# Kernel tuning notes

Hardware: AMD Instinct MI355X
Metric: run time of the kernel (lower is better)

The kernel has to match this reference:

```python
import jax, jax.numpy as jnp
import numpy as np

# Mamba defaults (mamba_ssm): d_state=16, d_conv=4, expand=2
D_MODEL = 256
D_STATE = 16
D_CONV = 4
D_INNER = 2 * D_MODEL          # expand * d_model = 512
DT_RANK = (D_MODEL + 15) // 16  # ceil(d_model/16) = 16
BATCH = 8
SEQLEN = 4096
LN_EPS = 1e-5


def setup_inputs() -> dict:
    key = jax.random.key(0)
    ks = jax.random.split(key, 8)
    s = lambda k, shape, sc=0.02: (jax.random.normal(k, shape, jnp.float32) * sc)
    return {
        "x": jax.random.normal(ks[0], (BATCH, SEQLEN, D_MODEL), jnp.float32),
        "in_proj_w": s(ks[1], (2 * D_INNER, D_MODEL)),
        "conv_w": s(ks[2], (D_INNER, 1, D_CONV), 0.1),
        "conv_b": jnp.zeros((D_INNER,), jnp.float32),
        "x_proj_w": s(ks[3], (DT_RANK + 2 * D_STATE, D_INNER)),
        "dt_proj_w": s(ks[4], (D_INNER, DT_RANK), 0.1),
        "dt_proj_b": s(ks[5], (D_INNER,), 0.1),
        "A_log": jnp.log(jnp.broadcast_to(
            jnp.arange(1, D_STATE + 1, dtype=jnp.float32), (D_INNER, D_STATE))),
        "D": jnp.ones((D_INNER,), jnp.float32),
        "out_proj_w": s(ks[6], (D_MODEL, D_INNER)),
        "ln_g": jnp.ones((D_MODEL,), jnp.float32),
        "ln_b": jnpps if False else jnp.zeros((D_MODEL,), jnp.float32),
    }


def _mamba_block(x, in_proj_w, conv_w, conv_b, x_proj_w, dt_proj_w, dt_proj_b,
                 A_log, D, out_proj_w, ln_g, ln_b):
    Bsz = x.shape[0]
    residual = x
    # input projection -> (u, z), each (B, L, d_inner)
    xz = jnp.einsum('bld,ed->ble', x, in_proj_w)
    u, z = jnp.split(xz, 2, axis=-1)
    # causal depthwise conv1d over time, then SiLU
    u_t = jnp.transpose(u, (0, 2, 1))                       # (B, d_inner, L)
    u_pad = jnp.pad(u_t, ((0, 0), (0, 0), (D_CONV - 1, 0)))
    u_conv = jax.lax.conv_general_dilated(
        u_pad, conv_w, window_strides=(1,), padding='VALID',
        feature_group_count=D_INNER) + conv_b[None, :, None]
    u_c = jax.nn.silu(jnp.transpose(u_conv, (0, 2, 1)))     # (B, L, d_inner)
    # input-dependent SSM parameters
    x_dbl = jnp.einsum('bld,ed->ble', u_c, x_proj_w)        # (B, L, dt_rank+2*d_state)
    dt, Bm, Cm = jnp.split(x_dbl, [DT_RANK, DT_RANK + D_STATE], axis=-1)
    delta = jax.nn.softplus(
        jnp.einsum('blr,dr->bld', dt, dt_proj_w) + dt_proj_b)  # (B, L, d_inner)
    A = -jnp.exp(A_log)                                     # (d_inner, d_state)

    def step(state, inputs):
        d_t, B_t, C_t, ut = inputs                          # (B,d_inner),(B,ds),(B,ds),(B,d_inner)
        dA = jnp.exp(d_t[..., None] * A)                    # (B, d_inner, d_state)
        state = state * dA + (d_t * ut)[..., None] * B_t[:, None, :]
        y_t = jnp.einsum('bds,bs->bd', state, C_t)
        return state, y_t

    init = jnp.zeros((Bsz, D_INNER, D_STATE), x.dtype)
    xs = (jnp.moveaxis(delta, 1, 0), jnp.moveaxis(Bm, 1, 0),
          jnp.moveaxis(Cm, 1, 0), jnp.moveaxis(u_c, 1, 0))
    _, ys = jax.lax.scan(step, init, xs)                    # (L, B, d_inner)
    y = jnp.moveaxis(ys, 0, 1) + u_c * D                    # skip term D*u
    y = y * jax.nn.silu(z)                                  # gating
    out = jnp.einsum('bld,ed->ble', y, out_proj_w)          # (B, L, d_model)
    # residual + LayerNorm (dropout is identity in eval)
    h = out + residual
    mu = jnp.mean(h, axis=-1, keepdims=True)
    var = jnp.var(h, axis=-1, keepdims=True)
    return (h - mu) * jax.lax.rsqrt(var + LN_EPS) * ln_g + ln_b


def reference(x, in_proj_w, conv_w, conv_b, x_proj_w, dt_proj_w, dt_proj_b,
              A_log, D, out_proj_w, ln_g, ln_b):
    return _mamba_block(x, in_proj_w, conv_w, conv_b, x_proj_w, dt_proj_w,
                        dt_proj_b, A_log, D, out_proj_w, ln_g, ln_b)
```

## Files before the change

### kernel.cpp

```cpp
#include <hip/hip_runtime.h>

typedef __bf16 bf16x8 __attribute__((ext_vector_type(8)));
typedef __bf16 bf16x4 __attribute__((ext_vector_type(4)));
typedef float f32x4 __attribute__((ext_vector_type(4)));

#define NC 128
#define CL 32

__global__ __launch_bounds__(256) void precomp_a2(
    const float* __restrict__ alog, float* __restrict__ A2)
{
  int i = blockIdx.x * 256 + threadIdx.x;
  int s = i >> 9, d = i & 511;
  A2[i] = -__expf(alog[d * 16 + s]) * 1.44269504f;
}

__global__ __launch_bounds__(256) void gemm_in(
    const float* __restrict__ A, const float* __restrict__ W,
    __bf16* __restrict__ o0, __bf16* __restrict__ o1,
    int K, int split, int ldo)
{
  __shared__ alignas(16) __bf16 lA[128 * 40];
  __shared__ alignas(16) __bf16 lB[128 * 40];
  const int tid  = threadIdx.x;
  const int m0   = blockIdx.x * 128;
  const int n0   = blockIdx.y * 128;
  const int wave = tid >> 6, lane = tid & 63;
  const int wr = (wave & 1) * 64, wc = (wave >> 1) * 64;
  const int fr = lane & 15, kh = (lane >> 4) * 8;
  const int srow = tid >> 3;
  const int skq  = (tid & 7) * 4;

  f32x4 acc[4][4] = {};

  for (int kt = 0; kt < K; kt += 32) {
    __syncthreads();
#pragma unroll
    for (int i = 0; i < 4; ++i) {
      int row = srow + i * 32;
      float4 va = *reinterpret_cast<const float4*>(A + (size_t)(m0 + row) * K + kt + skq);
      float4 vb = *reinterpret_cast<const float4*>(W + (size_t)(n0 + row) * K + kt + skq);
      bf16x4 pa = { (__bf16)va.x, (__bf16)va.y, (__bf16)va.z, (__bf16)va.w };
      bf16x4 pb = { (__bf16)vb.x, (__bf16)vb.y, (__bf16)vb.z, (__bf16)vb.w };
      *reinterpret_cast<bf16x4*>(&lA[row * 40 + skq]) = pa;
      *reinterpret_cast<bf16x4*>(&lB[row * 40 + skq]) = pb;
    }
    __syncthreads();
    bf16x8 af[4], bfr[4];
#pragma unroll
    for (int i = 0; i < 4; ++i) {
      af[i]  = *reinterpret_cast<const bf16x8*>(&lA[(wr + i * 16 + fr) * 40 + kh]);
      bfr[i] = *reinterpret_cast<const bf16x8*>(&lB[(wc + i * 16 + fr) * 40 + kh]);
    }
#pragma unroll
    for (int i = 0; i < 4; ++i)
#pragma unroll
      for (int j = 0; j < 4; ++j)
        acc[i][j] = __builtin_amdgcn_mfma_f32_16x16x32_bf16(af[i], bfr[j], acc[i][j], 0, 0, 0);
  }

  const int cr = (lane >> 4) * 4, cc = lane & 15;
#pragma unroll
  for (int i = 0; i < 4; ++i)
#pragma unroll
    for (int j = 0; j < 4; ++j)
#pragma unroll
      for (int r = 0; r < 4; ++r) {
        int m = m0 + wr + i * 16 + cr + r;
        int n = n0 + wc + j * 16 + cc;
        float v = acc[i][j][r];
        if (n < split) o0[(size_t)m * ldo + n] = (__bf16)v;
        else           o1[(size_t)m * ldo + (n - split)] = (__bf16)v;
      }
}

__global__ __launch_bounds__(256) void gemm_a16(
    const __bf16* __restrict__ A, const float* __restrict__ W,
    float* __restrict__ o)
{
  __shared__ alignas(16) __bf16 lA[128 * 40];
  __shared__ alignas(16) __bf16 lB[128 * 40];
  const int tid  = threadIdx.x;
  const int m0   = blockIdx.x * 128;
  const int n0   = blockIdx.y * 128;
  const int wave = tid >> 6, lane = tid & 63;
  const int wr = (wave & 1) * 64, wc = (wave >> 1) * 64;
  const int fr = lane & 15, kh = (lane >> 4) * 8;
  const int K = 512;

  f32x4 acc[4][4] = {};

  for (int kt = 0; kt < K; kt += 32) {
    __syncthreads();
#pragma unroll
    for (int i = 0; i < 2; ++i) {
      int row = (tid >> 2) + i * 64;
      int sk8 = (tid & 3) * 8;
      *reinterpret_cast<bf16x8*>(&lA[row * 40 + sk8]) =
          *reinterpret_cast<const bf16x8*>(A + (size_t)(m0 + row) * K + kt + sk8);
    }
#pragma unroll
    for (int i = 0; i < 4; ++i) {
      int row = (tid >> 3) + i * 32;
      int sk4 = (tid & 7) * 4;
      float4 vb = *reinterpret_cast<const float4*>(W + (size_t)(n0 + row) * K + kt + sk4);
      bf16x4 pb = { (__bf16)vb.x, (__bf16)vb.y, (__bf16)vb.z, (__bf16)vb.w };
      *reinterpret_cast<bf16x4*>(&lB[row * 40 + sk4]) = pb;
    }
    __syncthreads();
    bf16x8 af[4], bfr[4];
#pragma unroll
    for (int i = 0; i < 4; ++i) {
      af[i]  = *reinterpret_cast<const bf16x8*>(&lA[(wr + i * 16 + fr) * 40 + kh]);
      bfr[i] = *reinterpret_cast<const bf16x8*>(&lB[(wc + i * 16 + fr) * 40 + kh]);
    }
#pragma unroll
    for (int i = 0; i < 4; ++i)
#pragma unroll
      for (int j = 0; j < 4; ++j)
        acc[i][j] = __builtin_amdgcn_mfma_f32_16x16x32_bf16(af[i], bfr[j], acc[i][j], 0, 0, 0);
  }

  const int cr = (lane >> 4) * 4, cc = lane & 15;
#pragma unroll
  for (int i = 0; i < 4; ++i)
#pragma unroll
    for (int j = 0; j < 4; ++j)
#pragma unroll
      for (int r = 0; r < 4; ++r) {
        int m = m0 + wr + i * 16 + cr + r;
        int n = n0 + wc + j * 16 + cc;
        o[(size_t)m * 256 + n] = acc[i][j][r];
      }
}

__global__ __launch_bounds__(256) void gemm_n48(
    const __bf16* __restrict__ A, const float* __restrict__ W, float* __restrict__ o)
{
  __shared__ alignas(16) __bf16 lA[128 * 40];
  __shared__ alignas(16) __bf16 lB[48 * 40];
  const int tid  = threadIdx.x;
  const int m0   = blockIdx.x * 128;
  const int wave = tid >> 6, lane = tid & 63;
  const int wr = wave * 32;
  const int fr = lane & 15, kh = (lane >> 4) * 8;
  const int K = 512;

  f32x4 acc[2][3] = {};

  for (int kt = 0; kt < K; kt += 32) {
    __syncthreads();
#pragma unroll
    for (int i = 0; i < 2; ++i) {
      int row = (tid >> 2) + i * 64;
      int sk8 = (tid & 3) * 8;
      *reinterpret_cast<bf16x8*>(&lA[row * 40 + sk8]) =
          *reinterpret_cast<const bf16x8*>(A + (size_t)(m0 + row) * K + kt + sk8);
    }
#pragma unroll
    for (int i = 0; i < 2; ++i) {
      int slot = tid + i * 256;
      if (slot < 384) {
        int row = slot >> 3, kq = (slot & 7) * 4;
        float4 vb = *reinterpret_cast<const float4*>(W + (size_t)row * K + kt + kq);
        bf16x4 pb = { (__bf16)vb.x, (__bf16)vb.y, (__bf16)vb.z, (__bf16)vb.w };
        *reinterpret_cast<bf16x4*>(&lB[row * 40 + kq]) = pb;
      }
    }
    __syncthreads();
    bf16x8 af[2], bfr[3];
#pragma unroll
    for (int i = 0; i < 2; ++i)
      af[i] = *reinterpret_cast<const bf16x8*>(&lA[(wr + i * 16 + fr) * 40 + kh]);
#pragma unroll
    for (int j = 0; j < 3; ++j)
      bfr[j] = *reinterpret_cast<const bf16x8*>(&lB[(j * 16 + fr) * 40 + kh]);
#pragma unroll
    for (int i = 0; i < 2; ++i)
#pragma unroll
      for (int j = 0; j < 3; ++j)
        acc[i][j] = __builtin_amdgcn_mfma_f32_16x16x32_bf16(af[i], bfr[j], acc[i][j], 0, 0, 0);
  }

  const int cr = (lane >> 4) * 4, cc = lane & 15;
#pragma unroll
  for (int i = 0; i < 2; ++i)
#pragma unroll
    for (int j = 0; j < 3; ++j)
#pragma unroll
      for (int r = 0; r < 4; ++r) {
        int m = m0 + wr + i * 16 + cr + r;
        int n = j * 16 + cc;
        o[(size_t)m * 48 + n] = acc[i][j][r];
      }
}

__global__ __launch_bounds__(256) void conv_silu(
    const __bf16* __restrict__ u, const float* __restrict__ cw,
    const float* __restrict__ cb, __bf16* __restrict__ uc)
{
  int gid = blockIdx.x * 256 + threadIdx.x;
  int d8 = (gid & 63) * 8;
  int q  = gid >> 6;
  int t0 = (q & 1023) * 4;
  int b  = q >> 10;
  size_t base = ((size_t)b * 4096 + t0) * 512 + d8;
  float w0[8], w1[8], w2[8], w3[8], bias[8];
#pragma unroll
  for (int j = 0; j < 8; ++j) {
    float4 wv = *reinterpret_cast<const float4*>(cw + (d8 + j) * 4);
    w0[j] = wv.x; w1[j] = wv.y; w2[j] = wv.z; w3[j] = wv.w;
  }
  *reinterpret_cast<float4*>(&bias[0]) = *reinterpret_cast<const float4*>(cb + d8);
  *reinterpret_cast<float4*>(&bias[4]) = *reinterpret_cast<const float4*>(cb + d8 + 4);
  float x0[8], x1[8], x2[8];
#pragma unroll
  for (int j = 0; j < 8; ++j) { x0[j] = 0.f; x1[j] = 0.f; x2[j] = 0.f; }
  if (t0 > 0) {
    bf16x8 a = *reinterpret_cast<const bf16x8*>(u + base - 3 * 512);
    bf16x8 b2 = *reinterpret_cast<const bf16x8*>(u + base - 2 * 512);
    bf16x8 c = *reinterpret_cast<const bf16x8*>(u + base - 1 * 512);
#pragma unroll
    for (int j = 0; j < 8; ++j) { x0[j] = (float)a[j]; x1[j] = (float)b2[j]; x2[j] = (float)c[j]; }
  }
#pragma unroll
  for (int i = 0; i < 4; ++i) {
    bf16x8 v = *reinterpret_cast<const bf16x8*>(u + base + (size_t)i * 512);
    bf16x8 o;
#pragma unroll
    for (int j = 0; j < 8; ++j) {
      float x3 = (float)v[j];
      float a = fmaf(x3, w3[j], fmaf(x2[j], w2[j], fmaf(x1[j], w1[j], fmaf(x0[j], w0[j], bias[j]))));
      o[j] = (__bf16)(a / (1.f + __expf(-a)));
      x0[j] = x1[j]; x1[j] = x2[j]; x2[j] = x3;
    }
    *reinterpret_cast<bf16x8*>(uc + base + (size_t)i * 512) = o;
  }
}

__global__ __launch_bounds__(256) void scan_p1(
    const float* __restrict__ xdbl, const float* __restrict__ A2t,
    const float* __restrict__ dtw, const float* __restrict__ dtb,
    const float* __restrict__ Dv,
    __bf16* uc ,
    __bf16* __restrict__ cumb, float* __restrict__ hloc)
{
  const int bc = blockIdx.x;
  const int d  = blockIdx.y * 256 + threadIdx.x;
  const size_t row0 = (size_t)bc * CL;
  __shared__ float XD[CL * 48];
  for (int i = threadIdx.x; i < CL * 48; i += 256)
    XD[i] = xdbl[row0 * 48 + i];
  float w[16];
#pragma unroll
  for (int r = 0; r < 4; ++r) {
    float4 t4 = *reinterpret_cast<const float4*>(dtw + d * 16 + r * 4);
    w[r * 4] = t4.x; w[r * 4 + 1] = t4.y; w[r * 4 + 2] = t4.z; w[r * 4 + 3] = t4.w;
  }
  const float A2b  = A2t[d];
  const float bias = dtb[d];
  const float Dd   = Dv[d];
  __syncthreads();
  float st[16];
#pragma unroll
  for (int s = 0; s < 16; ++s) st[s] = 0.f;
  float cum = 0.f;
  for (int t = 0; t < CL; ++t) {
    size_t idx = (row0 + t) * 512 + d;
    float uv = (float)uc[idx];
    float a = bias;
#pragma unroll
    for (int r = 0; r < 16; ++r) a = fmaf(XD[t * 48 + r], w[r], a);
    float dl = fmaxf(a, 0.f) + __logf(1.f + __expf(-fabsf(a)));
    cum += dl;
    cumb[idx] = (__bf16)cum;
    float du = dl * uv;
    float r1 = __builtin_amdgcn_exp2f(dl * A2b);
    float r2 = r1 * r1;
    float r4 = r2 * r2;
    float e0 = r1, e1 = r2, e2 = r2 * r1, e3 = r4;
    float y0 = 0.f, y1 = 0.f, y2 = 0.f, y3 = 0.f;
#pragma unroll
    for (int sg = 0; sg < 4; ++sg) {
      int s0 = sg * 4;
      st[s0 + 0] = fmaf(st[s0 + 0], e0, du * XD[t * 48 + 16 + s0 + 0]);
      y0 = fmaf(st[s0 + 0], XD[t * 48 + 32 + s0 + 0], y0);
      st[s0 + 1] = fmaf(st[s0 + 1], e1, du * XD[t * 48 + 16 + s0 + 1]);
      y1 = fmaf(st[s0 + 1], XD[t * 48 + 32 + s0 + 1], y1);
      st[s0 + 2] = fmaf(st[s0 + 2], e2, du * XD[t * 48 + 16 + s0 + 2]);
      y2 = fmaf(st[s0 + 2], XD[t * 48 + 32 + s0 + 2], y2);
      st[s0 + 3] = fmaf(st[s0 + 3], e3, du * XD[t * 48 + 16 + s0 + 3]);
      y3 = fmaf(st[s0 + 3], XD[t * 48 + 32 + s0 + 3], y3);
      if (sg < 3) { e0 *= r4; e1 *= r4; e2 *= r4; e3 *= r4; }
    }
    uc[idx] = (__bf16)fmaf(uv, Dd, (y0 + y1) + (y2 + y3));
  }
#pragma unroll
  for (int s = 0; s < 16; ++s)
    hloc[((size_t)bc * 16 + s) * 512 + d] = st[s];
}

__global__ __launch_bounds__(256) void scan_p2(
    const float* __restrict__ A2t, const __bf16* __restrict__ cumb,
    float* hloc)
{
  int gt = blockIdx.x * 256 + threadIdx.x;
  int d = gt & 511, s = (gt >> 9) & 15, b = gt >> 13;
  float As2 = A2t[s * 512 + d];
  float st = 0.f;
  for (int c = 0; c < NC; ++c) {
    size_t bc = (size_t)b * NC + c;
    size_t hidx = (bc * 16 + s) * 512 + d;
    float h = hloc[hidx];
    hloc[hidx] = st;
    float ctot = (float)cumb[(bc * CL + CL - 1) * 512 + d];
    st = fmaf(st, __builtin_amdgcn_exp2f(As2 * ctot), h);
  }
}

__global__ __launch_bounds__(256) void scan_p3(
    const __bf16* __restrict__ z, const __bf16* __restrict__ cumb,
    const float* __restrict__ xdbl, const float* __restrict__ A2t,
    const float* __restrict__ sin_,
    __bf16* y )
{
  const int bc = blockIdx.x;
  const int d  = blockIdx.y * 256 + threadIdx.x;
  const size_t row0 = (size_t)bc * CL;
  __shared__ float Csh[CL * 16];
  for (int i = threadIdx.x; i < CL * 16; i += 256) {
    int tt = i >> 4, s = i & 15;
    Csh[i] = xdbl[(row0 + tt) * 48 + 32 + s];
  }
  const float A2b = A2t[d];
  float sn[16];
#pragma unroll
  for (int s = 0; s < 16; ++s) sn[s] = sin_[((size_t)bc * 16 + s) * 512 + d];
  __syncthreads();
  for (int t = 0; t < CL; ++t) {
    size_t idx = (row0 + t) * 512 + d;
    float cum = (float)cumb[idx];
    float yl  = (float)y[idx];
    float zv  = (float)z[idx];
    float R1 = __builtin_amdgcn_exp2f(cum * A2b);
    float R2 = R1 * R1;
    float R4 = R2 * R2;
    float e0 = R1, e1 = R2, e2 = R2 * R1, e3 = R4;
    float a0 = 0.f, a1 = 0.f, a2 = 0.f, a3 = 0.f;
#pragma unroll
    for (int sg = 0; sg < 4; ++sg) {
      int s0 = sg * 4;
      a0 = fmaf(sn[s0 + 0] * e0, Csh[t * 16 + s0 + 0], a0);
      a1 = fmaf(sn[s0 + 1] * e1, Csh[t * 16 + s0 + 1], a1);
      a2 = fmaf(sn[s0 + 2] * e2, Csh[t * 16 + s0 + 2], a2);
      a3 = fmaf(sn[s0 + 3] * e3, Csh[t * 16 + s0 + 3], a3);
      if (sg < 3) { e0 *= R4; e1 *= R4; e2 *= R4; e3 *= R4; }
    }
    float acc = yl + ((a0 + a1) + (a2 + a3));
    float g = zv / (1.f + __expf(-zv));
    y[idx] = (__bf16)(acc * g);
  }
}

__global__ __launch_bounds__(256) void ln_fuse(
    const float* om, const float* __restrict__ x,
    const float* __restrict__ g, const float* __restrict__ bta,
    float* out)
{
  const int row  = blockIdx.x * 4 + (threadIdx.x >> 6);
  const int lane = threadIdx.x & 63;
  const size_t base = (size_t)row * 256;
  float v[4];
  float s1 = 0.f, s2 = 0.f;
#pragma unroll
  for (int i = 0; i < 4; ++i) {
    float h = om[base + lane + i * 64] + x[base + lane + i * 64];
    v[i] = h; s1 += h; s2 = fmaf(h, h, s2);
  }
#pragma unroll
  for (int off = 32; off >= 1; off >>= 1) {
    s1 += __shfl_xor(s1, off);
    s2 += __shfl_xor(s2, off);
  }
  float mu  = s1 * (1.f / 256.f);
  float var = s2 * (1.f / 256.f) - mu * mu;
  float rs  = rsqrtf(var + 1e-5f);
#pragma unroll
  for (int i = 0; i < 4; ++i)
    out[base + lane + i * 64] = (v[i] - mu) * rs * g[lane + i * 64] + bta[lane + i * 64];
}

extern "C" void kernel_launch(void* const* d_in, const int* in_sizes, int n_in,
                              void* d_out, int out_size, void* d_ws, size_t ws_size,
                              hipStream_t stream) {
  const float* x    = (const float*)d_in[0];
  const float* ipw  = (const float*)d_in[1];
  const float* cw   = (const float*)d_in[2];
  const float* cb   = (const float*)d_in[3];
  const float* xpw  = (const float*)d_in[4];
  const float* dtw  = (const float*)d_in[5];
  const float* dtb  = (const float*)d_in[6];
  const float* alog = (const float*)d_in[7];
  const float* Dv   = (const float*)d_in[8];
  const float* opw  = (const float*)d_in[9];
  const float* lng  = (const float*)d_in[10];
  const float* lnb  = (const float*)d_in[11];
  float* out = (float*)d_out;

  float* ws = (float*)d_ws;
  __bf16* u_b   = (__bf16*)ws;
  __bf16* z_b   = (__bf16*)(ws + 8388608);
  __bf16* uc_b  = (__bf16*)(ws + 16777216);
  __bf16* cum_b = (__bf16*)(ws + 25165824);
  float* xdbl   = ws + 33554432;
  float* hloc   = ws + 35127296;
  float* A2     = ws + 43515904;

  precomp_a2<<<32, 256, 0, stream>>>(alog, A2);
  gemm_in<<<dim3(256, 8), 256, 0, stream>>>(x, ipw, u_b, z_b, 256, 512, 512);
  conv_silu<<<2048, 256, 0, stream>>>(u_b, cw, cb, uc_b);
  gemm_n48<<<256, 256, 0, stream>>>(uc_b, xpw, xdbl);
  scan_p1<<<dim3(8 * NC, 2), 256, 0, stream>>>(xdbl, A2, dtw, dtb, Dv, uc_b, cum_b, hloc);
  scan_p2<<<256, 256, 0, stream>>>(A2, cum_b, hloc);
  scan_p3<<<dim3(8 * NC, 2), 256, 0, stream>>>(z_b, cum_b, xdbl, A2, hloc, uc_b);
  gemm_a16<<<dim3(256, 2), 256, 0, stream>>>(uc_b, opw, out);
  ln_fuse<<<8192, 256, 0, stream>>>(out, x, lng, lnb, out);
}
```

Baseline: 236.7 us.

## Move delta projection to MFMA GEMM, pack scan math, swap GEMM grid order

A new MFMA kernel computes delta = softplus(dt @ dt_proj_w^T + bias) in bf16 ahead of time. It reuses the u buffer, which is dead after the conv. This removes the per-thread 16-wide dot product and softplus from the serial scan_p1 loop. scan_p1 and scan_p3 now use two-wide float vectors so the compiler can emit packed FP32 math. scan_p2 reads per-chunk delta sums from a new fp32 array instead of the bf16 cumulative value. The in and out GEMMs swap blockIdx x/y so blocks that share the same A rows run together, for cache reuse. The cost is an extra kernel launch, a round trip of delta through memory, and delta rounded to bf16.

```diff
diff --git a/kernel.cpp b/kernel.cpp
--- a/kernel.cpp
+++ b/kernel.cpp
@@ -3,6 +3,7 @@
 typedef __bf16 bf16x8 __attribute__((ext_vector_type(8)));
 typedef __bf16 bf16x4 __attribute__((ext_vector_type(4)));
 typedef float f32x4 __attribute__((ext_vector_type(4)));
+typedef float f32x2 __attribute__((ext_vector_type(2)));
 
 #define NC 128
 #define CL 32
@@ -23,8 +24,8 @@
   __shared__ alignas(16) __bf16 lA[128 * 40];
   __shared__ alignas(16) __bf16 lB[128 * 40];
   const int tid  = threadIdx.x;
-  const int m0   = blockIdx.x * 128;
-  const int n0   = blockIdx.y * 128;
+  const int m0   = blockIdx.y * 128;
+  const int n0   = blockIdx.x * 128;
   const int wave = tid >> 6, lane = tid & 63;
   const int wr = (wave & 1) * 64, wc = (wave >> 1) * 64;
   const int fr = lane & 15, kh = (lane >> 4) * 8;
@@ -81,8 +82,8 @@
   __shared__ alignas(16) __bf16 lA[128 * 40];
   __shared__ alignas(16) __bf16 lB[128 * 40];
   const int tid  = threadIdx.x;
-  const int m0   = blockIdx.x * 128;
-  const int n0   = blockIdx.y * 128;
+  const int m0   = blockIdx.y * 128;
+  const int n0   = blockIdx.x * 128;
   const int wave = tid >> 6, lane = tid & 63;
   const int wr = (wave & 1) * 64, wc = (wave >> 1) * 64;
   const int fr = lane & 15, kh = (lane >> 4) * 8;
@@ -195,6 +196,67 @@
       }
 }
 
+__global__ __launch_bounds__(256) void gemm_delta(
+    const float* __restrict__ xdbl, const float* __restrict__ dtw,
+    const float* __restrict__ dtb, __bf16* __restrict__ delta)
+{
+  __shared__ alignas(16) __bf16 lA[128 * 40];
+  __shared__ alignas(16) __bf16 lB[128 * 40];
+  const int tid = threadIdx.x;
+  const int n0 = blockIdx.x * 128;
+  const int m0 = blockIdx.y * 128;
+  const int wave = tid >> 6, lane = tid & 63;
+  const int wr = (wave & 1) * 64, wc = (wave >> 1) * 64;
+  const int fr = lane & 15, kh = (lane >> 4) * 8;
+
+  {
+    int row = tid >> 1, h = (tid & 1) * 8;
+    float4 v0 = *reinterpret_cast<const float4*>(xdbl + (size_t)(m0 + row) * 48 + h);
+    float4 v1 = *reinterpret_cast<const float4*>(xdbl + (size_t)(m0 + row) * 48 + h + 4);
+    bf16x8 pa = { (__bf16)v0.x, (__bf16)v0.y, (__bf16)v0.z, (__bf16)v0.w,
+                  (__bf16)v1.x, (__bf16)v1.y, (__bf16)v1.z, (__bf16)v1.w };
+    bf16x8 zz = {};
+    *reinterpret_cast<bf16x8*>(&lA[row * 40 + h]) = pa;
+    *reinterpret_cast<bf16x8*>(&lA[row * 40 + 16 + h]) = zz;
+    float4 w0 = *reinterpret_cast<const float4*>(dtw + (size_t)(n0 + row) * 16 + h);
+    float4 w1 = *reinterpret_cast<const float4*>(dtw + (size_t)(n0 + row) * 16 + h + 4);
+    bf16x8 pb = { (__bf16)w0.x, (__bf16)w0.y, (__bf16)w0.z, (__bf16)w0.w,
+                  (__bf16)w1.x, (__bf16)w1.y, (__bf16)w1.z, (__bf16)w1.w };
+    *reinterpret_cast<bf16x8*>(&lB[row * 40 + h]) = pb;
+    *reinterpret_cast<bf16x8*>(&lB[row * 40 + 16 + h]) = zz;
+  }
+  __syncthreads();
+
+  f32x4 acc[4][4] = {};
+  bf16x8 af[4], bfr[4];
+#pragma unroll
+  for (int i = 0; i < 4; ++i) {
+    af[i]  = *reinterpret_cast<const bf16x8*>(&lA[(wr + i * 16 + fr) * 40 + kh]);
+    bfr[i] = *reinterpret_cast<const bf16x8*>(&lB[(wc + i * 16 + fr) * 40 + kh]);
+  }
+#pragma unroll
+  for (int i = 0; i < 4; ++i)
+#pragma unroll
+    for (int j = 0; j < 4; ++j)
+      acc[i][j] = __builtin_amdgcn_mfma_f32_16x16x32_bf16(af[i], bfr[j], acc[i][j], 0, 0, 0);
+
+  const int cr = (lane >> 4) * 4, cc = lane & 15;
+#pragma unroll
+  for (int j = 0; j < 4; ++j) {
+    int n = n0 + wc + j * 16 + cc;
+    float bias = dtb[n];
+#pragma unroll
+    for (int i = 0; i < 4; ++i)
+#pragma unroll
+      for (int r = 0; r < 4; ++r) {
+        int m = m0 + wr + i * 16 + cr + r;
+        float a = acc[i][j][r] + bias;
+        float sp = fmaxf(a, 0.f) + __logf(1.f + __expf(-fabsf(a)));
+        delta[(size_t)m * 512 + n] = (__bf16)sp;
+      }
+  }
+}
+
 __global__ __launch_bounds__(256) void conv_silu(
     const __bf16* __restrict__ u, const float* __restrict__ cw,
     const float* __restrict__ cb, __bf16* __restrict__ uc)
@@ -240,68 +302,67 @@
 
 __global__ __launch_bounds__(256) void scan_p1(
     const float* __restrict__ xdbl, const float* __restrict__ A2t,
-    const float* __restrict__ dtw, const float* __restrict__ dtb,
-    const float* __restrict__ Dv,
+    const __bf16* __restrict__ delta, const float* __restrict__ Dv,
     __bf16* uc ,
-    __bf16* __restrict__ cumb, float* __restrict__ hloc)
+    __bf16* __restrict__ cumb, float* __restrict__ dsum,
+    float* __restrict__ hloc)
 {
   const int bc = blockIdx.x;
   const int d  = blockIdx.y * 256 + threadIdx.x;
   const size_t row0 = (size_t)bc * CL;
-  __shared__ float XD[CL * 48];
-  for (int i = threadIdx.x; i < CL * 48; i += 256)
-    XD[i] = xdbl[row0 * 48 + i];
-  float w[16];
-#pragma unroll
-  for (int r = 0; r < 4; ++r) {
-    float4 t4 = *reinterpret_cast<const float4*>(dtw + d * 16 + r * 4);
-    w[r * 4] = t4.x; w[r * 4 + 1] = t4.y; w[r * 4 + 2] = t4.z; w[r * 4 + 3] = t4.w;
-  }
-  const float A2b  = A2t[d];
-  const float bias = dtb[d];
-  const float Dd   = Dv[d];
+  __shared__ float XD[CL * 32];
+  for (int i = threadIdx.x; i < CL * 32; i += 256) {
+    int tt = i >> 5, s = i & 31;
+    XD[i] = xdbl[(row0 + tt) * 48 + 16 + s];
+  }
+  const float A2b = A2t[d];
+  const float Dd  = Dv[d];
   __syncthreads();
-  float st[16];
-#pragma unroll
-  for (int s = 0; s < 16; ++s) st[s] = 0.f;
+  f32x2 st[8];
+#pragma unroll
+  for (int p = 0; p < 8; ++p) { f32x2 zz = {0.f, 0.f}; st[p] = zz; }
   float cum = 0.f;
   for (int t = 0; t < CL; ++t) {
     size_t idx = (row0 + t) * 512 + d;
+    float dl = (float)delta[idx];
     float uv = (float)uc[idx];
-    float a = bias;
-#pragma unroll
-    for (int r = 0; r < 16; ++r) a = fmaf(XD[t * 48 + r], w[r], a);
-    float dl = fmaxf(a, 0.f) + __logf(1.f + __expf(-fabsf(a)));
     cum += dl;
     cumb[idx] = (__bf16)cum;
     float du = dl * uv;
+    f32x2 du2 = {du, du};
     float r1 = __builtin_amdgcn_exp2f(dl * A2b);
-    float r2 = r1 * r1;
-    float r4 = r2 * r2;
-    float e0 = r1, e1 = r2, e2 = r2 * r1, e3 = r4;
-    float y0 = 0.f, y1 = 0.f, y2 = 0.f, y3 = 0.f;
+    float r2 = r1 * r1, r4 = r2 * r2;
+    f32x2 eA = {r1, r2};
+    f32x2 eB = {r2 * r1, r4};
+    f32x2 r4v = {r4, r4};
+    f32x2 ya = {0.f, 0.f}, yb = {0.f, 0.f};
 #pragma unroll
     for (int sg = 0; sg < 4; ++sg) {
-      int s0 = sg * 4;
-      st[s0 + 0] = fmaf(st[s0 + 0], e0, du * XD[t * 48 + 16 + s0 + 0]);
-      y0 = fmaf(st[s0 + 0], XD[t * 48 + 32 + s0 + 0], y0);
-      st[s0 + 1] = fmaf(st[s0 + 1], e1, du * XD[t * 48 + 16 + s0 + 1]);
-      y1 = fmaf(st[s0 + 1], XD[t * 48 + 32 + s0 + 1], y1);
-      st[s0 + 2] = fmaf(st[s0 + 2], e2, du * XD[t * 48 + 16 + s0 + 2]);
-      y2 = fmaf(st[s0 + 2], XD[t * 48 + 32 + s0 + 2], y2);
-      st[s0 + 3] = fmaf(st[s0 + 3], e3, du * XD[t * 48 + 16 + s0 + 3]);
-      y3 = fmaf(st[s0 + 3], XD[t * 48 + 32 + s0 + 3], y3);
-      if (sg < 3) { e0 *= r4; e1 *= r4; e2 *= r4; e3 *= r4; }
-    }
-    uc[idx] = (__bf16)fmaf(uv, Dd, (y0 + y1) + (y2 + y3));
-  }
-#pragma unroll
-  for (int s = 0; s < 16; ++s)
-    hloc[((size_t)bc * 16 + s) * 512 + d] = st[s];
+      f32x4 B4 = *reinterpret_cast<const f32x4*>(&XD[t * 32 + sg * 4]);
+      f32x4 C4 = *reinterpret_cast<const f32x4*>(&XD[t * 32 + 16 + sg * 4]);
+      f32x2 B0 = __builtin_shufflevector(B4, B4, 0, 1);
+      f32x2 B1 = __builtin_shufflevector(B4, B4, 2, 3);
+      f32x2 C0 = __builtin_shufflevector(C4, C4, 0, 1);
+      f32x2 C1 = __builtin_shufflevector(C4, C4, 2, 3);
+      st[sg * 2]     = st[sg * 2]     * eA + du2 * B0;
+      st[sg * 2 + 1] = st[sg * 2 + 1] * eB + du2 * B1;
+      ya = ya + st[sg * 2] * C0;
+      yb = yb + st[sg * 2 + 1] * C1;
+      if (sg < 3) { eA = eA * r4v; eB = eB * r4v; }
+    }
+    float y = (ya.x + ya.y) + (yb.x + yb.y);
+    uc[idx] = (__bf16)fmaf(uv, Dd, y);
+  }
+  dsum[(size_t)bc * 512 + d] = cum;
+#pragma unroll
+  for (int p = 0; p < 8; ++p) {
+    hloc[((size_t)bc * 16 + 2 * p) * 512 + d]     = st[p].x;
+    hloc[((size_t)bc * 16 + 2 * p + 1) * 512 + d] = st[p].y;
+  }
 }
 
 __global__ __launch_bounds__(256) void scan_p2(
-    const float* __restrict__ A2t, const __bf16* __restrict__ cumb,
+    const float* __restrict__ A2t, const float* __restrict__ dsum,
     float* hloc)
 {
   int gt = blockIdx.x * 256 + threadIdx.x;
@@ -313,8 +374,7 @@
     size_t hidx = (bc * 16 + s) * 512 + d;
     float h = hloc[hidx];
     hloc[hidx] = st;
-    float ctot = (float)cumb[(bc * CL + CL - 1) * 512 + d];
-    st = fmaf(st, __builtin_amdgcn_exp2f(As2 * ctot), h);
+    st = fmaf(st, __builtin_amdgcn_exp2f(As2 * dsum[bc * 512 + d]), h);
   }
 }
 
@@ -333,9 +393,13 @@
     Csh[i] = xdbl[(row0 + tt) * 48 + 32 + s];
   }
   const float A2b = A2t[d];
-  float sn[16];
-#pragma unroll
-  for (int s = 0; s < 16; ++s) sn[s] = sin_[((size_t)bc * 16 + s) * 512 + d];
+  f32x2 sn[8];
+#pragma unroll
+  for (int p = 0; p < 8; ++p) {
+    f32x2 v = { sin_[((size_t)bc * 16 + 2 * p) * 512 + d],
+                sin_[((size_t)bc * 16 + 2 * p + 1) * 512 + d] };
+    sn[p] = v;
+  }
   __syncthreads();
   for (int t = 0; t < CL; ++t) {
     size_t idx = (row0 + t) * 512 + d;
@@ -343,20 +407,21 @@
     float yl  = (float)y[idx];
     float zv  = (float)z[idx];
     float R1 = __builtin_amdgcn_exp2f(cum * A2b);
-    float R2 = R1 * R1;
-    float R4 = R2 * R2;
-    float e0 = R1, e1 = R2, e2 = R2 * R1, e3 = R4;
-    float a0 = 0.f, a1 = 0.f, a2 = 0.f, a3 = 0.f;
+    float R2 = R1 * R1, R4 = R2 * R2;
+    f32x2 eA = {R1, R2};
+    f32x2 eB = {R2 * R1, R4};
+    f32x2 R4v = {R4, R4};
+    f32x2 aa = {0.f, 0.f}, ab = {0.f, 0.f};
 #pragma unroll
     for (int sg = 0; sg < 4; ++sg) {
-      int s0 = sg * 4;
-      a0 = fmaf(sn[s0 + 0] * e0, Csh[t * 16 + s0 + 0], a0);
-      a1 = fmaf(sn[s0 + 1] * e1, Csh[t * 16 + s0 + 1], a1);
-      a2 = fmaf(sn[s0 + 2] * e2, Csh[t * 16 + s0 + 2], a2);
-      a3 = fmaf(sn[s0 + 3] * e3, Csh[t * 16 + s0 + 3], a3);
-      if (sg < 3) { e0 *= R4; e1 *= R4; e2 *= R4; e3 *= R4; }
-    }
-    float acc = yl + ((a0 + a1) + (a2 + a3));
+      f32x4 C4 = *reinterpret_cast<const f32x4*>(&Csh[t * 16 + sg * 4]);
+      f32x2 C0 = __builtin_shufflevector(C4, C4, 0, 1);
+      f32x2 C1 = __builtin_shufflevector(C4, C4, 2, 3);
+      aa = aa + (sn[sg * 2] * eA) * C0;
+      ab = ab + (sn[sg * 2 + 1] * eB) * C1;
+      if (sg < 3) { eA = eA * R4v; eB = eB * R4v; }
+    }
+    float acc = yl + (aa.x + aa.y) + (ab.x + ab.y);
     float g = zv / (1.f + __expf(-zv));
     y[idx] = (__bf16)(acc * g);
   }
@@ -415,14 +480,17 @@
   float* xdbl   = ws + 33554432;
   float* hloc   = ws + 35127296;
   float* A2     = ws + 43515904;
+  float* dsum   = ws + 43524096;
+  __bf16* dlt_b = u_b;
 
   precomp_a2<<<32, 256, 0, stream>>>(alog, A2);
-  gemm_in<<<dim3(256, 8), 256, 0, stream>>>(x, ipw, u_b, z_b, 256, 512, 512);
+  gemm_in<<<dim3(8, 256), 256, 0, stream>>>(x, ipw, u_b, z_b, 256, 512, 512);
   conv_silu<<<2048, 256, 0, stream>>>(u_b, cw, cb, uc_b);
   gemm_n48<<<256, 256, 0, stream>>>(uc_b, xpw, xdbl);
-  scan_p1<<<dim3(8 * NC, 2), 256, 0, stream>>>(xdbl, A2, dtw, dtb, Dv, uc_b, cum_b, hloc);
-  scan_p2<<<256, 256, 0, stream>>>(A2, cum_b, hloc);
+  gemm_delta<<<dim3(4, 256), 256, 0, stream>>>(xdbl, dtw, dtb, dlt_b);
+  scan_p1<<<dim3(8 * NC, 2), 256, 0, stream>>>(xdbl, A2, dlt_b, Dv, uc_b, cum_b, dsum, hloc);
+  scan_p2<<<256, 256, 0, stream>>>(A2, dsum, hloc);
   scan_p3<<<dim3(8 * NC, 2), 256, 0, stream>>>(z_b, cum_b, xdbl, A2, hloc, uc_b);
-  gemm_a16<<<dim3(256, 2), 256, 0, stream>>>(uc_b, opw, out);
+  gemm_a16<<<dim3(2, 256), 256, 0, stream>>>(uc_b, opw, out);
   ln_fuse<<<8192, 256, 0, stream>>>(out, x, lng, lnb, out);
 }
```

After: 246.4 us. 1.04x slower.
